# Performance work log

Hardware: AMD Instinct MI355X
Metric: run time of the kernel (lower is better)

The kernel has to match this reference:

```python
import jax, jax.numpy as jnp
import numpy as np

B, N, DIM, H, DH = 4, 2048, 1024, 16, 64  # batch, seq, model dim, heads, head dim


def setup_inputs() -> dict:
    key = jax.random.key(0)
    k1, k2, k3 = jax.random.split(key, 3)
    x = jax.random.normal(k1, (B, N, DIM), dtype=jnp.float32)
    w_qkv = jax.random.normal(k2, (DIM, 3 * H * DH), dtype=jnp.float32) * (DIM ** -0.5)
    w_out = jax.random.normal(k3, (H * DH, DIM), dtype=jnp.float32) * ((H * DH) ** -0.5)
    b_out = jnp.zeros((DIM,), dtype=jnp.float32)
    return {"x": x, "w_qkv": w_qkv, "w_out": w_out, "b_out": b_out}


def reference(x, w_qkv, w_out, b_out):
    scale = DH ** -0.5
    qkv = x @ w_qkv                              # [b, n, 3*h*d]
    q, k, v = jnp.split(qkv, 3, axis=-1)
    # 'b n (h d) -> b h n d'
    def to_heads(t):
        return t.reshape(B, N, H, DH).transpose(0, 2, 1, 3)
    q, k, v = to_heads(q), to_heads(k), to_heads(v)
    dots = jnp.einsum('bhid,bhjd->bhij', q, k) * scale   # [b, h, n, n]
    attn = jax.nn.softmax(dots, axis=-1)
    out = jnp.einsum('bhij,bhjd->bhid', attn, v)          # [b, h, n, d]
    out = out.transpose(0, 2, 1, 3).reshape(B, N, H * DH) # 'b h n d -> b n (h d)'
    return out @ w_out + b_out
```

## Files before the change

### kernel.cpp

```cpp
#include <hip/hip_runtime.h>
#include <stdint.h>

#define B_    4
#define N_    2048
#define DIM_  1024
#define H_    16
#define DH_   64
#define BN_   (B_ * N_)
#define QKVN_ (3 * H_ * DH_)

#define AS1_ __attribute__((address_space(1)))
#define AS3_ __attribute__((address_space(3)))

typedef unsigned short u16;
typedef __attribute__((ext_vector_type(8))) __bf16 bf16x8;
typedef __attribute__((ext_vector_type(8))) short  short8;
typedef __attribute__((ext_vector_type(4))) float  f32x4;
typedef __attribute__((ext_vector_type(4))) u16    u16x4;

__device__ inline u16 f2bf(float f) {
    union { __bf16 b; u16 u; } v; v.b = (__bf16)f; return v.u;
}
__device__ inline float bf2f(u16 u) {
    union { uint32_t u; float f; } v; v.u = ((uint32_t)u) << 16;
    return v.f;
}

__global__ __launch_bounds__(256) void cast_f32_bf16(const float* __restrict__ in,
                                                     u16* __restrict__ out, int n4) {
    int i = blockIdx.x * blockDim.x + threadIdx.x;
    int stride = gridDim.x * blockDim.x;
    for (; i < n4; i += stride) {
        float4 v = reinterpret_cast<const float4*>(in)[i];
        u16x4 o;
        o.x = f2bf(v.x); o.y = f2bf(v.y); o.z = f2bf(v.z); o.w = f2bf(v.w);
        reinterpret_cast<u16x4*>(out)[i] = o;
    }
}

__global__ __launch_bounds__(256) void transpose_cast(const float* __restrict__ in,
                                                      u16* __restrict__ out, int R, int C) {
    int gid = blockIdx.x * blockDim.x + threadIdx.x;
    int total = C * (R / 4);
    if (gid >= total) return;
    int n  = gid % C;
    int k4 = (gid / C) * 4;
    u16x4 o;
    o.x = f2bf(in[(size_t)(k4 + 0) * C + n]);
    o.y = f2bf(in[(size_t)(k4 + 1) * C + n]);
    o.z = f2bf(in[(size_t)(k4 + 2) * C + n]);
    o.w = f2bf(in[(size_t)(k4 + 3) * C + n]);
    *reinterpret_cast<u16x4*>(&out[(size_t)n * R + k4]) = o;
}

template <bool BF16_OUT>
__global__ __launch_bounds__(256) void gemm_bt(const u16* __restrict__ A,
                                               const u16* __restrict__ BT,
                                               void* __restrict__ Cout,
                                               const float* __restrict__ bias,
                                               int M, int Nn, int K) {
    __shared__ __align__(16) u16 AsF[128 * 32];
    __shared__ __align__(16) u16 BsF[128 * 32];

    const int tid  = threadIdx.x;
    const int m0   = blockIdx.y * 128;
    const int n0   = blockIdx.x * 128;
    const int w    = tid >> 6;
    const int lane = tid & 63;
    const int lr   = lane & 15;
    const int lg   = lane >> 4;
    const int wm   = w >> 1;
    const int wn   = w & 1;

    f32x4 acc[4][4] = {};

    const int sr = tid >> 2;
    const int sc = (tid & 3) * 8;
    const u16* Aptr = A  + (size_t)(m0 + sr) * K + sc;
    const u16* Bptr = BT + (size_t)(n0 + sr) * K + sc;
    const int ldsb = w * 512;

    for (int kt = 0; kt < K; kt += 32) {
        __builtin_amdgcn_global_load_lds((const AS1_ void*)(Aptr + kt),
                                         (AS3_ void*)&AsF[ldsb], 16, 0, 0);
        __builtin_amdgcn_global_load_lds((const AS1_ void*)(Aptr + (size_t)64 * K + kt),
                                         (AS3_ void*)&AsF[2048 + ldsb], 16, 0, 0);
        __builtin_amdgcn_global_load_lds((const AS1_ void*)(Bptr + kt),
                                         (AS3_ void*)&BsF[ldsb], 16, 0, 0);
        __builtin_amdgcn_global_load_lds((const AS1_ void*)(Bptr + (size_t)64 * K + kt),
                                         (AS3_ void*)&BsF[2048 + ldsb], 16, 0, 0);
        __syncthreads();

        bf16x8 af[4], bfr[4];
#pragma unroll
        for (int m = 0; m < 4; m++)
            af[m] = *reinterpret_cast<const bf16x8*>(&AsF[(wm * 64 + m * 16 + lr) * 32 + lg * 8]);
#pragma unroll
        for (int n = 0; n < 4; n++)
            bfr[n] = *reinterpret_cast<const bf16x8*>(&BsF[(wn * 64 + n * 16 + lr) * 32 + lg * 8]);
#pragma unroll
        for (int m = 0; m < 4; m++)
#pragma unroll
            for (int n = 0; n < 4; n++)
                acc[m][n] = __builtin_amdgcn_mfma_f32_16x16x32_bf16(af[m], bfr[n], acc[m][n], 0, 0, 0);
        __syncthreads();
    }

#pragma unroll
    for (int m = 0; m < 4; m++)
#pragma unroll
        for (int n = 0; n < 4; n++) {
            const int row = m0 + wm * 64 + m * 16 + lg * 4;
            const int col = n0 + wn * 64 + n * 16 + lr;
#pragma unroll
            for (int r = 0; r < 4; r++) {
                if (BF16_OUT) {
                    ((u16*)Cout)[(size_t)(row + r) * Nn + col] = f2bf(acc[m][n][r]);
                } else {
                    ((float*)Cout)[(size_t)(row + r) * Nn + col] = acc[m][n][r] + bias[col];
                }
            }
        }
}

__global__ __launch_bounds__(256) void attn_kernel(const u16* __restrict__ qkv,
                                                   u16* __restrict__ out) {
    __shared__ __align__(16) u16      Ks[2][64][40];
    __shared__ __align__(16) uint32_t VT32[64 * 36];
    __shared__ __align__(16) u16      Ps[4][16][72];

    const int tid  = threadIdx.x;
    const int w    = tid >> 6;
    const int lane = tid & 63;
    const int lr   = lane & 15;
    const int lg   = lane >> 4;

    const int bh = blockIdx.y;
    const int b  = bh >> 4;
    const int h  = bh & 15;
    const int rowbase = b * N_;
    const int q0 = blockIdx.x * 64;
    const int qoff = h * DH_;

    bf16x8 qf[2];
    {
        const float qscale = 0.125f * 1.4426950408889634f;
        const int qrow = rowbase + q0 + w * 16 + lr;
#pragma unroll
        for (int ks = 0; ks < 2; ks++) {
            short8 raw = *reinterpret_cast<const short8*>(
                &qkv[(size_t)qrow * QKVN_ + qoff + ks * 32 + lg * 8]);
            const u16* ru = reinterpret_cast<const u16*>(&raw);
            union { u16 u[8]; bf16x8 v; } q;
#pragma unroll
            for (int j = 0; j < 8; j++) q.u[j] = f2bf(bf2f(ru[j]) * qscale);
            qf[ks] = q.v;
        }
    }

    float mrun = -3e38f, lrun = 0.f;
    f32x4 acc_o[4] = {};

    const u16* kg = qkv + (size_t)rowbase * QKVN_ + DIM_ + qoff;
    const u16* vg = qkv + (size_t)rowbase * QKVN_ + 2 * DIM_ + qoff;

    const int kr = tid >> 2;
    const int kc = (tid & 3) * 8;
    const size_t koff0 = (size_t)kr * QKVN_ + kc;
    const int vp  = tid >> 3;
    const int vsc = (tid & 7) * 8;
    const size_t voff0 = (size_t)(vp * 2) * QKVN_ + vsc;
    const size_t voff1 = voff0 + QKVN_;

    int vb_off[2][4];
#pragma unroll
    for (int c = 0; c < 2; c++)
#pragma unroll
        for (int n = 0; n < 4; n++) {
            const int d = n * 16 + lr;
            vb_off[c][n] = d * 36 + ((c * 16 + lg * 4) ^ (((d >> 2) & 7) << 2));
        }

    short8 kst[2], vst[2];
    kst[0] = *reinterpret_cast<const short8*>(kg + koff0);
    kst[1] = *reinterpret_cast<const short8*>(kg + koff0 + 32);
    vst[0] = *reinterpret_cast<const short8*>(vg + voff0);
    vst[1] = *reinterpret_cast<const short8*>(vg + voff1);

    *reinterpret_cast<short8*>(&Ks[0][kr][kc]) = kst[0];
    *reinterpret_cast<short8*>(&Ks[1][kr][kc]) = kst[1];
    {
        const u16* v0 = reinterpret_cast<const u16*>(&vst[0]);
        const u16* v1 = reinterpret_cast<const u16*>(&vst[1]);
#pragma unroll
        for (int i = 0; i < 8; i++) {
            const int d = vsc + i;
            const int col = vp ^ (((d >> 2) & 7) << 2);
            VT32[d * 36 + col] = (uint32_t)v0[i] | ((uint32_t)v1[i] << 16);
        }
    }
    __syncthreads();

    for (int t = 0; t < N_ / 64; t++) {
        if (t + 1 < N_ / 64) {
            const u16* kg2 = kg + (size_t)(t + 1) * 64 * QKVN_;
            const u16* vg2 = vg + (size_t)(t + 1) * 64 * QKVN_;
            kst[0] = *reinterpret_cast<const short8*>(kg2 + koff0);
            kst[1] = *reinterpret_cast<const short8*>(kg2 + koff0 + 32);
            vst[0] = *reinterpret_cast<const short8*>(vg2 + voff0);
            vst[1] = *reinterpret_cast<const short8*>(vg2 + voff1);
        }

        f32x4 s[4];
#pragma unroll
        for (int n = 0; n < 4; n++) {
            bf16x8 k0 = *reinterpret_cast<const bf16x8*>(&Ks[0][n * 16 + lr][lg * 8]);
            bf16x8 k1 = *reinterpret_cast<const bf16x8*>(&Ks[1][n * 16 + lr][lg * 8]);
            f32x4 z = {0.f, 0.f, 0.f, 0.f};
            s[n] = __builtin_amdgcn_mfma_f32_16x16x32_bf16(k0, qf[0], z, 0, 0, 0);
            s[n] = __builtin_amdgcn_mfma_f32_16x16x32_bf16(k1, qf[1], s[n], 0, 0, 0);
        }

        float tmax = fmaxf(fmaxf(s[0][0], s[0][1]), fmaxf(s[0][2], s[0][3]));
#pragma unroll
        for (int n = 1; n < 4; n++)
            tmax = fmaxf(tmax, fmaxf(fmaxf(s[n][0], s[n][1]), fmaxf(s[n][2], s[n][3])));
        tmax = fmaxf(tmax, __shfl_xor(tmax, 16));
        tmax = fmaxf(tmax, __shfl_xor(tmax, 32));

        if (!__all(tmax - mrun <= 8.f)) {
            float mnew = fmaxf(mrun, tmax);
            float fac  = exp2f(mrun - mnew);
            mrun = mnew;
            lrun *= fac;
            float facq[4];
#pragma unroll
            for (int r = 0; r < 4; r++) facq[r] = __shfl(fac, (lane & 48) | (lg * 4 + r));
#pragma unroll
            for (int n = 0; n < 4; n++)
#pragma unroll
                for (int r = 0; r < 4; r++) acc_o[n][r] *= facq[r];
        }

        float psum = 0.f;
#pragma unroll
        for (int n = 0; n < 4; n++) {
            float p0 = exp2f(s[n][0] - mrun);
            float p1 = exp2f(s[n][1] - mrun);
            float p2 = exp2f(s[n][2] - mrun);
            float p3 = exp2f(s[n][3] - mrun);
            psum += (p0 + p1) + (p2 + p3);
            u16x4 pw;
            pw.x = f2bf(p0); pw.y = f2bf(p1); pw.z = f2bf(p2); pw.w = f2bf(p3);
            *reinterpret_cast<u16x4*>(&Ps[w][lr][n * 16 + lg * 4]) = pw;
        }
        psum += __shfl_xor(psum, 16);
        psum += __shfl_xor(psum, 32);
        lrun += psum;

#pragma unroll
        for (int c = 0; c < 2; c++) {
            bf16x8 pa = *reinterpret_cast<const bf16x8*>(&Ps[w][lr][c * 32 + lg * 8]);
#pragma unroll
            for (int n = 0; n < 4; n++) {
                bf16x8 vf = *reinterpret_cast<const bf16x8*>(&VT32[vb_off[c][n]]);
                acc_o[n] = __builtin_amdgcn_mfma_f32_16x16x32_bf16(pa, vf, acc_o[n], 0, 0, 0);
            }
        }

        __syncthreads();
        if (t + 1 < N_ / 64) {
            *reinterpret_cast<short8*>(&Ks[0][kr][kc]) = kst[0];
            *reinterpret_cast<short8*>(&Ks[1][kr][kc]) = kst[1];
            const u16* v0 = reinterpret_cast<const u16*>(&vst[0]);
            const u16* v1 = reinterpret_cast<const u16*>(&vst[1]);
#pragma unroll
            for (int i = 0; i < 8; i++) {
                const int d = vsc + i;
                const int col = vp ^ (((d >> 2) & 7) << 2);
                VT32[d * 36 + col] = (uint32_t)v0[i] | ((uint32_t)v1[i] << 16);
            }
        }
        __syncthreads();
    }

    float linv = 1.f / lrun;
    float lq[4];
#pragma unroll
    for (int r = 0; r < 4; r++) lq[r] = __shfl(linv, (lane & 48) | (lg * 4 + r));
#pragma unroll
    for (int n = 0; n < 4; n++)
#pragma unroll
        for (int r = 0; r < 4; r++) {
            const int row = rowbase + q0 + w * 16 + lg * 4 + r;
            const int col = qoff + n * 16 + lr;
            out[(size_t)row * DIM_ + col] = f2bf(acc_o[n][r] * lq[r]);
        }
}

extern "C" void kernel_launch(void* const* d_in, const int* in_sizes, int n_in,
                              void* d_out, int out_size, void* d_ws, size_t ws_size,
                              hipStream_t stream) {
    const float* x     = (const float*)d_in[0];
    const float* w_qkv = (const float*)d_in[1];
    const float* w_out = (const float*)d_in[2];
    const float* b_out = (const float*)d_in[3];
    float* out = (float*)d_out;

    char* ws = (char*)d_ws;
    u16* xbf   = (u16*)(ws);
    u16* wqkvT = (u16*)(ws + 16777216);
    u16* woutT = (u16*)(ws + 23068672);
    u16* qkv   = (u16*)(ws + 25165824);
    u16* attnO = (u16*)(ws + 75497472);

    cast_f32_bf16<<<2048, 256, 0, stream>>>(x, xbf, (BN_ * DIM_) / 4);
    transpose_cast<<<(DIM_ / 4) * QKVN_ / 256, 256, 0, stream>>>(w_qkv, wqkvT, DIM_, QKVN_);
    transpose_cast<<<(DIM_ / 4) * DIM_ / 256, 256, 0, stream>>>(w_out, woutT, DIM_, DIM_);

    gemm_bt<true><<<dim3(QKVN_ / 128, BN_ / 128), 256, 0, stream>>>(
        xbf, wqkvT, qkv, nullptr, BN_, QKVN_, DIM_);

    attn_kernel<<<dim3(N_ / 64, B_ * H_), 256, 0, stream>>>(qkv, attnO);

    gemm_bt<false><<<dim3(DIM_ / 128, BN_ / 128), 256, 0, stream>>>(
        attnO, woutT, out, b_out, BN_, DIM_, DIM_);
}
```

Before: 351.8 us.

## Rewrite attention kernel with 32x32 MFMA and 128-query blocks

The attention kernel now uses 32x32x16 MFMA tiles, with each wave handling 32 queries so a block covers 128 queries. This halves the grid and doubles the reuse of each K/V tile loaded into shared memory. The softmax scale is applied in the exp step through an FMA instead of pre-scaling Q, so the row max and sum need fewer cross-lane shuffles. It also changes the XOR swizzles for K, V and P and writes the output as vectorized stores, at the cost of more registers per thread and fewer blocks to hide latency.

```diff
diff --git a/kernel.cpp b/kernel.cpp
--- a/kernel.cpp
+++ b/kernel.cpp
@@ -13,10 +13,11 @@
 #define AS3_ __attribute__((address_space(3)))
 
 typedef unsigned short u16;
-typedef __attribute__((ext_vector_type(8))) __bf16 bf16x8;
-typedef __attribute__((ext_vector_type(8))) short  short8;
-typedef __attribute__((ext_vector_type(4))) float  f32x4;
-typedef __attribute__((ext_vector_type(4))) u16    u16x4;
+typedef __attribute__((ext_vector_type(8)))  __bf16 bf16x8;
+typedef __attribute__((ext_vector_type(8)))  short  short8;
+typedef __attribute__((ext_vector_type(4)))  float  f32x4;
+typedef __attribute__((ext_vector_type(16))) float  f32x16;
+typedef __attribute__((ext_vector_type(4)))  u16    u16x4;
 
 __device__ inline u16 f2bf(float f) {
     union { __bf16 b; u16 u; } v; v.b = (__bf16)f; return v.u;
@@ -125,79 +126,76 @@
 
 __global__ __launch_bounds__(256) void attn_kernel(const u16* __restrict__ qkv,
                                                    u16* __restrict__ out) {
-    __shared__ __align__(16) u16      Ks[2][64][40];
-    __shared__ __align__(16) uint32_t VT32[64 * 36];
-    __shared__ __align__(16) u16      Ps[4][16][72];
+    __shared__ __align__(16) u16      KsS[64 * 64];
+    __shared__ __align__(16) uint32_t VTs[64 * 32];
+    __shared__ __align__(16) uint32_t PsW[4 * 32 * 36];
 
     const int tid  = threadIdx.x;
     const int w    = tid >> 6;
     const int lane = tid & 63;
-    const int lr   = lane & 15;
-    const int lg   = lane >> 4;
+    const int q32  = lane & 31;
+    const int hi   = lane >> 5;
 
     const int bh = blockIdx.y;
     const int b  = bh >> 4;
     const int h  = bh & 15;
     const int rowbase = b * N_;
-    const int q0 = blockIdx.x * 64;
-    const int qoff = h * DH_;
-
-    bf16x8 qf[2];
+    const int qglob = blockIdx.x * 128 + w * 32 + q32;
+    const int qoff  = h * DH_;
+    const float qs = 0.125f * 1.4426950408889634f;
+
+    bf16x8 qf[4];
     {
-        const float qscale = 0.125f * 1.4426950408889634f;
-        const int qrow = rowbase + q0 + w * 16 + lr;
-#pragma unroll
-        for (int ks = 0; ks < 2; ks++) {
-            short8 raw = *reinterpret_cast<const short8*>(
-                &qkv[(size_t)qrow * QKVN_ + qoff + ks * 32 + lg * 8]);
-            const u16* ru = reinterpret_cast<const u16*>(&raw);
-            union { u16 u[8]; bf16x8 v; } q;
-#pragma unroll
-            for (int j = 0; j < 8; j++) q.u[j] = f2bf(bf2f(ru[j]) * qscale);
-            qf[ks] = q.v;
-        }
-    }
+        const u16* qp = qkv + (size_t)(rowbase + qglob) * QKVN_ + qoff;
+#pragma unroll
+        for (int ks = 0; ks < 4; ks++)
+            qf[ks] = *reinterpret_cast<const bf16x8*>(qp + ks * 16 + hi * 8);
+    }
+
+    int kch[4], vrd[4];
+#pragma unroll
+    for (int ks = 0; ks < 4; ks++) {
+        kch[ks] = ((2 * ks + hi) ^ (q32 & 7)) * 8;
+        vrd[ks] = (ks * 8 + hi * 4) ^ ((q32 & 7) << 2);
+    }
+    const int krowA = q32 * 64;
+    const int krowB = (32 + q32) * 64;
+    const int vrowA = q32 * 32;
+    const int vrowB = (32 + q32) * 32;
+    const int psw   = w * 1152 + q32 * 36;
+    const int pswW  = psw + 2 * hi;
+    const int pswR  = psw + 4 * hi;
 
     float mrun = -3e38f, lrun = 0.f;
-    f32x4 acc_o[4] = {};
+    f32x16 o0, o1;
+#pragma unroll
+    for (int r = 0; r < 16; r++) { o0[r] = 0.f; o1[r] = 0.f; }
 
     const u16* kg = qkv + (size_t)rowbase * QKVN_ + DIM_ + qoff;
     const u16* vg = qkv + (size_t)rowbase * QKVN_ + 2 * DIM_ + qoff;
 
-    const int kr = tid >> 2;
-    const int kc = (tid & 3) * 8;
-    const size_t koff0 = (size_t)kr * QKVN_ + kc;
-    const int vp  = tid >> 3;
-    const int vsc = (tid & 7) * 8;
-    const size_t voff0 = (size_t)(vp * 2) * QKVN_ + vsc;
-    const size_t voff1 = voff0 + QKVN_;
-
-    int vb_off[2][4];
-#pragma unroll
-    for (int c = 0; c < 2; c++)
-#pragma unroll
-        for (int n = 0; n < 4; n++) {
-            const int d = n * 16 + lr;
-            vb_off[c][n] = d * 36 + ((c * 16 + lg * 4) ^ (((d >> 2) & 7) << 2));
-        }
-
-    short8 kst[2], vst[2];
-    kst[0] = *reinterpret_cast<const short8*>(kg + koff0);
-    kst[1] = *reinterpret_cast<const short8*>(kg + koff0 + 32);
-    vst[0] = *reinterpret_cast<const short8*>(vg + voff0);
-    vst[1] = *reinterpret_cast<const short8*>(vg + voff1);
-
-    *reinterpret_cast<short8*>(&Ks[0][kr][kc]) = kst[0];
-    *reinterpret_cast<short8*>(&Ks[1][kr][kc]) = kst[1];
+    const int kr = tid >> 2, ka = tid & 3;
+    const size_t kgo = (size_t)kr * QKVN_ + ka * 16;
+    const int kl0 = kr * 64 + ((2 * ka)     ^ (kr & 7)) * 8;
+    const int kl1 = kr * 64 + ((2 * ka + 1) ^ (kr & 7)) * 8;
+    const int vp = tid >> 3, vd = (tid & 7) * 8;
+    const size_t vgo0 = (size_t)(2 * vp) * QKVN_ + vd;
+    const size_t vgo1 = vgo0 + QKVN_;
+
+    short8 kst0, kst1, vst0, vst1;
+    kst0 = *reinterpret_cast<const short8*>(kg + kgo);
+    kst1 = *reinterpret_cast<const short8*>(kg + kgo + 8);
+    vst0 = *reinterpret_cast<const short8*>(vg + vgo0);
+    vst1 = *reinterpret_cast<const short8*>(vg + vgo1);
+
+    *reinterpret_cast<short8*>(&KsS[kl0]) = kst0;
+    *reinterpret_cast<short8*>(&KsS[kl1]) = kst1;
     {
-        const u16* v0 = reinterpret_cast<const u16*>(&vst[0]);
-        const u16* v1 = reinterpret_cast<const u16*>(&vst[1]);
-#pragma unroll
-        for (int i = 0; i < 8; i++) {
-            const int d = vsc + i;
-            const int col = vp ^ (((d >> 2) & 7) << 2);
-            VT32[d * 36 + col] = (uint32_t)v0[i] | ((uint32_t)v1[i] << 16);
-        }
+        const u16* v0 = reinterpret_cast<const u16*>(&vst0);
+        const u16* v1 = reinterpret_cast<const u16*>(&vst1);
+#pragma unroll
+        for (int i = 0; i < 8; i++)
+            VTs[(vd + i) * 32 + (vp ^ (i << 2))] = (uint32_t)v0[i] | ((uint32_t)v1[i] << 16);
     }
     __syncthreads();
 
@@ -205,97 +203,104 @@
         if (t + 1 < N_ / 64) {
             const u16* kg2 = kg + (size_t)(t + 1) * 64 * QKVN_;
             const u16* vg2 = vg + (size_t)(t + 1) * 64 * QKVN_;
-            kst[0] = *reinterpret_cast<const short8*>(kg2 + koff0);
-            kst[1] = *reinterpret_cast<const short8*>(kg2 + koff0 + 32);
-            vst[0] = *reinterpret_cast<const short8*>(vg2 + voff0);
-            vst[1] = *reinterpret_cast<const short8*>(vg2 + voff1);
-        }
-
-        f32x4 s[4];
-#pragma unroll
-        for (int n = 0; n < 4; n++) {
-            bf16x8 k0 = *reinterpret_cast<const bf16x8*>(&Ks[0][n * 16 + lr][lg * 8]);
-            bf16x8 k1 = *reinterpret_cast<const bf16x8*>(&Ks[1][n * 16 + lr][lg * 8]);
-            f32x4 z = {0.f, 0.f, 0.f, 0.f};
-            s[n] = __builtin_amdgcn_mfma_f32_16x16x32_bf16(k0, qf[0], z, 0, 0, 0);
-            s[n] = __builtin_amdgcn_mfma_f32_16x16x32_bf16(k1, qf[1], s[n], 0, 0, 0);
-        }
-
-        float tmax = fmaxf(fmaxf(s[0][0], s[0][1]), fmaxf(s[0][2], s[0][3]));
-#pragma unroll
-        for (int n = 1; n < 4; n++)
-            tmax = fmaxf(tmax, fmaxf(fmaxf(s[n][0], s[n][1]), fmaxf(s[n][2], s[n][3])));
-        tmax = fmaxf(tmax, __shfl_xor(tmax, 16));
+            kst0 = *reinterpret_cast<const short8*>(kg2 + kgo);
+            kst1 = *reinterpret_cast<const short8*>(kg2 + kgo + 8);
+            vst0 = *reinterpret_cast<const short8*>(vg2 + vgo0);
+            vst1 = *reinterpret_cast<const short8*>(vg2 + vgo1);
+        }
+
+        f32x16 sa0, sa1;
+#pragma unroll
+        for (int r = 0; r < 16; r++) { sa0[r] = 0.f; sa1[r] = 0.f; }
+#pragma unroll
+        for (int ks = 0; ks < 4; ks++) {
+            bf16x8 a0 = *reinterpret_cast<const bf16x8*>(&KsS[krowA + kch[ks]]);
+            bf16x8 a1 = *reinterpret_cast<const bf16x8*>(&KsS[krowB + kch[ks]]);
+            sa0 = __builtin_amdgcn_mfma_f32_32x32x16_bf16(a0, qf[ks], sa0, 0, 0, 0);
+            sa1 = __builtin_amdgcn_mfma_f32_32x32x16_bf16(a1, qf[ks], sa1, 0, 0, 0);
+        }
+
+        float tmax = sa0[0];
+#pragma unroll
+        for (int r = 1; r < 16; r++) tmax = fmaxf(tmax, sa0[r]);
+#pragma unroll
+        for (int r = 0; r < 16; r++) tmax = fmaxf(tmax, sa1[r]);
         tmax = fmaxf(tmax, __shfl_xor(tmax, 32));
-
-        if (!__all(tmax - mrun <= 8.f)) {
-            float mnew = fmaxf(mrun, tmax);
+        const float ts = tmax * qs;
+
+        if (!__all(ts - mrun <= 8.f)) {
+            float mnew = fmaxf(mrun, ts);
             float fac  = exp2f(mrun - mnew);
             mrun = mnew;
             lrun *= fac;
-            float facq[4];
-#pragma unroll
-            for (int r = 0; r < 4; r++) facq[r] = __shfl(fac, (lane & 48) | (lg * 4 + r));
-#pragma unroll
-            for (int n = 0; n < 4; n++)
-#pragma unroll
-                for (int r = 0; r < 4; r++) acc_o[n][r] *= facq[r];
+#pragma unroll
+            for (int r = 0; r < 16; r++) { o0[r] *= fac; o1[r] *= fac; }
         }
 
         float psum = 0.f;
 #pragma unroll
-        for (int n = 0; n < 4; n++) {
-            float p0 = exp2f(s[n][0] - mrun);
-            float p1 = exp2f(s[n][1] - mrun);
-            float p2 = exp2f(s[n][2] - mrun);
-            float p3 = exp2f(s[n][3] - mrun);
-            psum += (p0 + p1) + (p2 + p3);
-            u16x4 pw;
-            pw.x = f2bf(p0); pw.y = f2bf(p1); pw.z = f2bf(p2); pw.w = f2bf(p3);
-            *reinterpret_cast<u16x4*>(&Ps[w][lr][n * 16 + lg * 4]) = pw;
-        }
-        psum += __shfl_xor(psum, 16);
+        for (int r = 0; r < 16; r++) {
+            sa0[r] = exp2f(__builtin_fmaf(sa0[r], qs, -mrun));
+            psum += sa0[r];
+        }
+#pragma unroll
+        for (int r = 0; r < 16; r++) {
+            sa1[r] = exp2f(__builtin_fmaf(sa1[r], qs, -mrun));
+            psum += sa1[r];
+        }
         psum += __shfl_xor(psum, 32);
         lrun += psum;
 
 #pragma unroll
-        for (int c = 0; c < 2; c++) {
-            bf16x8 pa = *reinterpret_cast<const bf16x8*>(&Ps[w][lr][c * 32 + lg * 8]);
-#pragma unroll
-            for (int n = 0; n < 4; n++) {
-                bf16x8 vf = *reinterpret_cast<const bf16x8*>(&VT32[vb_off[c][n]]);
-                acc_o[n] = __builtin_amdgcn_mfma_f32_16x16x32_bf16(pa, vf, acc_o[n], 0, 0, 0);
-            }
+        for (int j = 0; j < 4; j++) {
+            u16x4 pw;
+            pw.x = f2bf(sa0[4 * j + 0]); pw.y = f2bf(sa0[4 * j + 1]);
+            pw.z = f2bf(sa0[4 * j + 2]); pw.w = f2bf(sa0[4 * j + 3]);
+            *reinterpret_cast<u16x4*>(&PsW[pswW + 4 * j]) = pw;
+        }
+#pragma unroll
+        for (int j = 0; j < 4; j++) {
+            u16x4 pw;
+            pw.x = f2bf(sa1[4 * j + 0]); pw.y = f2bf(sa1[4 * j + 1]);
+            pw.z = f2bf(sa1[4 * j + 2]); pw.w = f2bf(sa1[4 * j + 3]);
+            *reinterpret_cast<u16x4*>(&PsW[pswW + 16 + 4 * j]) = pw;
+        }
+
+#pragma unroll
+        for (int ks = 0; ks < 4; ks++) {
+            bf16x8 pb  = *reinterpret_cast<const bf16x8*>(&PsW[pswR + ks * 8]);
+            bf16x8 va0 = *reinterpret_cast<const bf16x8*>(&VTs[vrowA + vrd[ks]]);
+            bf16x8 va1 = *reinterpret_cast<const bf16x8*>(&VTs[vrowB + vrd[ks]]);
+            o0 = __builtin_amdgcn_mfma_f32_32x32x16_bf16(va0, pb, o0, 0, 0, 0);
+            o1 = __builtin_amdgcn_mfma_f32_32x32x16_bf16(va1, pb, o1, 0, 0, 0);
         }
 
         __syncthreads();
         if (t + 1 < N_ / 64) {
-            *reinterpret_cast<short8*>(&Ks[0][kr][kc]) = kst[0];
-            *reinterpret_cast<short8*>(&Ks[1][kr][kc]) = kst[1];
-            const u16* v0 = reinterpret_cast<const u16*>(&vst[0]);
-            const u16* v1 = reinterpret_cast<const u16*>(&vst[1]);
-#pragma unroll
-            for (int i = 0; i < 8; i++) {
-                const int d = vsc + i;
-                const int col = vp ^ (((d >> 2) & 7) << 2);
-                VT32[d * 36 + col] = (uint32_t)v0[i] | ((uint32_t)v1[i] << 16);
-            }
+            *reinterpret_cast<short8*>(&KsS[kl0]) = kst0;
+            *reinterpret_cast<short8*>(&KsS[kl1]) = kst1;
+            const u16* v0 = reinterpret_cast<const u16*>(&vst0);
+            const u16* v1 = reinterpret_cast<const u16*>(&vst1);
+#pragma unroll
+            for (int i = 0; i < 8; i++)
+                VTs[(vd + i) * 32 + (vp ^ (i << 2))] = (uint32_t)v0[i] | ((uint32_t)v1[i] << 16);
         }
         __syncthreads();
     }
 
-    float linv = 1.f / lrun;
-    float lq[4];
-#pragma unroll
-    for (int r = 0; r < 4; r++) lq[r] = __shfl(linv, (lane & 48) | (lg * 4 + r));
-#pragma unroll
-    for (int n = 0; n < 4; n++)
-#pragma unroll
-        for (int r = 0; r < 4; r++) {
-            const int row = rowbase + q0 + w * 16 + lg * 4 + r;
-            const int col = qoff + n * 16 + lr;
-            out[(size_t)row * DIM_ + col] = f2bf(acc_o[n][r] * lq[r]);
-        }
+    const float linv = 1.f / lrun;
+    u16* orow = out + (size_t)(rowbase + qglob) * DIM_ + qoff;
+#pragma unroll
+    for (int j = 0; j < 4; j++) {
+        u16x4 ov;
+        ov.x = f2bf(o0[4 * j + 0] * linv); ov.y = f2bf(o0[4 * j + 1] * linv);
+        ov.z = f2bf(o0[4 * j + 2] * linv); ov.w = f2bf(o0[4 * j + 3] * linv);
+        *reinterpret_cast<u16x4*>(&orow[8 * j + 4 * hi]) = ov;
+        u16x4 ow;
+        ow.x = f2bf(o1[4 * j + 0] * linv); ow.y = f2bf(o1[4 * j + 1] * linv);
+        ow.z = f2bf(o1[4 * j + 2] * linv); ow.w = f2bf(o1[4 * j + 3] * linv);
+        *reinterpret_cast<u16x4*>(&orow[32 + 8 * j + 4 * hi]) = ow;
+    }
 }
 
 extern "C" void kernel_launch(void* const* d_in, const int* in_sizes, int n_in,
@@ -321,7 +326,7 @@
     gemm_bt<true><<<dim3(QKVN_ / 128, BN_ / 128), 256, 0, stream>>>(
         xbf, wqkvT, qkv, nullptr, BN_, QKVN_, DIM_);
 
-    attn_kernel<<<dim3(N_ / 64, B_ * H_), 256, 0, stream>>>(qkv, attnO);
+    attn_kernel<<<dim3(N_ / 128, B_ * H_), 256, 0, stream>>>(qkv, attnO);
 
     gemm_bt<false><<<dim3(DIM_ / 128, BN_ / 128), 256, 0, stream>>>(
         attnO, woutT, out, b_out, BN_, DIM_, DIM_);
```

Measured after the change: 346.7 us. About the same (-1.5%).
